# Kernel optimization log

Hardware: AMD Instinct MI355X
Metric: run time of the kernel (lower is better)

Reference implementation:

```python
import jax, jax.numpy as jnp
import numpy as np

EPS = 1e-6
GROUPS = 8


def setup_inputs() -> dict:
    key = jax.random.key(0)
    ks = jax.random.split(key, 8)
    B, C, H, W = 4, 128, 64, 64
    s = 1.0 / np.sqrt(C)
    return {
        "x": jax.random.normal(ks[0], (B, C, H, W), jnp.float32),
        "gn_scale": jnp.ones((C,), jnp.float32),
        "gn_bias": jnp.zeros((C,), jnp.float32),
        "wq": jax.random.normal(ks[1], (C, C), jnp.float32) * s,
        "bq": jnp.zeros((C,), jnp.float32),
        "wk": jax.random.normal(ks[2], (C, C), jnp.float32) * s,
        "bk": jnp.zeros((C,), jnp.float32),
        "wv": jax.random.normal(ks[3], (C, C), jnp.float32) * s,
        "bv": jnp.zeros((C,), jnp.float32),
        "wp": jax.random.normal(ks[4], (C, C), jnp.float32) * s,
        "bp": jnp.zeros((C,), jnp.float32),
    }


def _group_norm(x, scale, bias):
    B, C, H, W = x.shape
    g = x.reshape(B, GROUPS, C // GROUPS, H * W)
    mu = g.mean(axis=(2, 3), keepdims=True)
    var = g.var(axis=(2, 3), keepdims=True)
    g = (g - mu) * jax.lax.rsqrt(var + EPS)
    g = g.reshape(B, C, H, W)
    return g * scale[None, :, None, None] + bias[None, :, None, None]


def reference(x, gn_scale, gn_bias, wq, bq, wk, bk, wv, bv, wp, bp):
    B, C, H, W = x.shape
    N = H * W
    h = _group_norm(x, gn_scale, gn_bias).reshape(B, C, N)
    # 1x1 convs == channel matmuls: (C_out, C_in) x (B, C_in, N)
    q = jnp.einsum('oc,bcn->bon', wq, h) + bq[None, :, None]
    k = jnp.einsum('oc,bcn->bon', wk, h) + bk[None, :, None]
    v = jnp.einsum('oc,bcn->bon', wv, h) + bv[None, :, None]
    # scores: (B, N, N), w[b,n,m] = sum_c q[b,c,n] k[b,c,m]
    w = jnp.einsum('bcn,bcm->bnm', q, k) * (C ** -0.5)
    w = jax.nn.softmax(w, axis=-1)
    # h_[b,c,n] = sum_m w[b,n,m] v[b,c,m]
    h_ = jnp.einsum('bnm,bcm->bcn', w, v)
    out = jnp.einsum('oc,bcn->bon', wp, h_) + bp[None, :, None]
    return x + out.reshape(B, C, H, W)
```

## Files before the change

kernel.cpp:

```cpp
#include <hip/hip_runtime.h>
#include <math.h>

#define B_ 4
#define C_ 128
#define N_ 4096
#define NSPLIT 4
#define MT 32
#define PLD 40
#define HLD 136
#define VTLD 24

typedef float floatx4 __attribute__((ext_vector_type(4)));
typedef short bf16x8 __attribute__((ext_vector_type(8)));

__device__ __forceinline__ ushort f2bf(float f) {
  unsigned u = __float_as_uint(f);
  return (ushort)((u + 0x7FFF + ((u >> 16) & 1)) >> 16);
}
__device__ __forceinline__ float bf2f(ushort u) {
  return __uint_as_float(((unsigned)u) << 16);
}
__device__ __forceinline__ unsigned pkbf(float a, float b) {
  return __builtin_amdgcn_perm(__float_as_uint(a) + 0x8000u,
                               __float_as_uint(b) + 0x8000u, 0x07060302u);
}
__device__ __forceinline__ void gl2lds16(const ushort* g, ushort* l) {
  __builtin_amdgcn_global_load_lds(
      (const __attribute__((address_space(1))) void*)g,
      (__attribute__((address_space(3))) void*)l, 16, 0, 0);
}

__global__ __launch_bounds__(256) void prep_kernel(
    const float* __restrict__ x, float* __restrict__ gstat,
    const float* __restrict__ wq, const float* __restrict__ wk,
    const float* __restrict__ wv, const float* __restrict__ wp,
    ushort* __restrict__ wB) {
  if (blockIdx.x >= 256) {
    int i = (blockIdx.x - 256) * 256 + threadIdx.x;
    int m = i >> 14, j = i & 16383;
    const float* src = (m == 0) ? wq : (m == 1) ? wk : (m == 2) ? wv : wp;
    wB[i] = f2bf(src[j]);
    return;
  }
  int b = blockIdx.x >> 6, g = (blockIdx.x >> 3) & 7, part = blockIdx.x & 7;
  const float4* xp = (const float4*)(x + (size_t)(b * C_ + g * 16) * N_) + part * 2048;
  float s = 0.f, ss = 0.f;
  for (int i = threadIdx.x; i < 2048; i += 256) {
    float4 v = xp[i];
    s += v.x + v.y + v.z + v.w;
    ss += v.x * v.x + v.y * v.y + v.z * v.z + v.w * v.w;
  }
  #pragma unroll
  for (int o = 32; o > 0; o >>= 1) {
    s += __shfl_down(s, o, 64);
    ss += __shfl_down(ss, o, 64);
  }
  __shared__ float rs[4], rss[4];
  int wid = threadIdx.x >> 6, lane = threadIdx.x & 63;
  if (lane == 0) { rs[wid] = s; rss[wid] = ss; }
  __syncthreads();
  if (threadIdx.x == 0) {
    int slot = (b * 8 + g) * 8 + part;
    gstat[slot]       = rs[0] + rs[1] + rs[2] + rs[3];
    gstat[256 + slot] = rss[0] + rss[1] + rss[2] + rss[3];
  }
}

__global__ __launch_bounds__(256) void gnqkv_kernel(
    const float* __restrict__ x, const float* __restrict__ gstat,
    const float* __restrict__ scale, const float* __restrict__ bias,
    const ushort* __restrict__ wB,
    const float* __restrict__ bq, const float* __restrict__ bk,
    const float* __restrict__ bv,
    ushort* __restrict__ qT, ushort* __restrict__ kT, ushort* __restrict__ vB) {
  __shared__ __align__(16) ushort hs[16][HLD];
  __shared__ __align__(16) ushort Qt[16][HLD];
  __shared__ __align__(16) ushort Kt[16][HLD];
  __shared__ __align__(16) ushort Vt[128][VTLD];
  __shared__ float sSc[C_], sBi[C_];
  int tid = threadIdx.x;
  int b = blockIdx.x >> 8;
  int n0 = (blockIdx.x & 255) * 16;
  if (tid < 128) {
    int g = tid >> 4;
    float S = 0.f, SS = 0.f;
    #pragma unroll
    for (int p = 0; p < 8; ++p) {
      S  += gstat[(b * 8 + g) * 8 + p];
      SS += gstat[256 + (b * 8 + g) * 8 + p];
    }
    float mu = S * (1.f / 65536.f);
    float var = SS * (1.f / 65536.f) - mu * mu;
    float rstd = rsqrtf(var + 1e-6f);
    float sc = scale[tid] * rstd;
    sSc[tid] = sc;
    sBi[tid] = bias[tid] - mu * sc;
  }
  __syncthreads();
  #pragma unroll
  for (int k2 = 0; k2 < 2; ++k2) {
    int i = tid + k2 * 256;
    int c = i >> 2, n4 = i & 3;
    float4 v = *(const float4*)(x + (size_t)(b * C_ + c) * N_ + n0 + n4 * 4);
    float sc = sSc[c], bi = sBi[c];
    hs[n4 * 4 + 0][c] = f2bf(v.x * sc + bi);
    hs[n4 * 4 + 1][c] = f2bf(v.y * sc + bi);
    hs[n4 * 4 + 2][c] = f2bf(v.z * sc + bi);
    hs[n4 * 4 + 3][c] = f2bf(v.w * sc + bi);
  }
  __syncthreads();
  int lane = tid & 63, w = tid >> 6;
  int col = lane & 15, quad = lane >> 4;
  int oh = w * 32;
  bf16x8 hf[4];
  #pragma unroll
  for (int kc = 0; kc < 4; ++kc)
    hf[kc] = *(const bf16x8*)&hs[col][kc * 32 + quad * 8];
  const ushort* Wq = wB;
  const ushort* Wk = wB + 16384;
  const ushort* Wv = wB + 32768;
  const float scl = 0.12751879752224991f;
  #pragma unroll
  for (int ot = 0; ot < 2; ++ot) {
    int o0 = oh + ot * 16;
    floatx4 aq = (floatx4)0.f, ak = (floatx4)0.f, av = (floatx4)0.f;
    #pragma unroll
    for (int kc = 0; kc < 4; ++kc) {
      int wo = (o0 + col) * C_ + kc * 32 + quad * 8;
      aq = __builtin_amdgcn_mfma_f32_16x16x32_bf16(*(const bf16x8*)&Wq[wo], hf[kc], aq, 0, 0, 0);
      ak = __builtin_amdgcn_mfma_f32_16x16x32_bf16(*(const bf16x8*)&Wk[wo], hf[kc], ak, 0, 0, 0);
      av = __builtin_amdgcn_mfma_f32_16x16x32_bf16(*(const bf16x8*)&Wv[wo], hf[kc], av, 0, 0, 0);
    }
    float4 bqv = *(const float4*)&bq[o0 + quad * 4];
    float4 bkv = *(const float4*)&bk[o0 + quad * 4];
    float4 bvv = *(const float4*)&bv[o0 + quad * 4];
    uint2 qs = { pkbf((aq[1] + bqv.y) * scl, (aq[0] + bqv.x) * scl),
                 pkbf((aq[3] + bqv.w) * scl, (aq[2] + bqv.z) * scl) };
    uint2 ks = { pkbf(ak[1] + bkv.y, ak[0] + bkv.x),
                 pkbf(ak[3] + bkv.w, ak[2] + bkv.z) };
    *(uint2*)&Qt[col][o0 + quad * 4] = qs;
    *(uint2*)&Kt[col][o0 + quad * 4] = ks;
    float vv[4] = {av[0] + bvv.x, av[1] + bvv.y, av[2] + bvv.z, av[3] + bvv.w};
    #pragma unroll
    for (int r = 0; r < 4; ++r)
      Vt[o0 + quad * 4 + r][col] = f2bf(vv[r]);
  }
  __syncthreads();
  {
    int row = tid >> 4, seg = tid & 15;
    size_t dst = ((size_t)b * N_ + n0 + row) * C_ + seg * 8;
    *(uint4*)(qT + dst) = *(const uint4*)&Qt[row][seg * 8];
    *(uint4*)(kT + dst) = *(const uint4*)&Kt[row][seg * 8];
  }
  {
    int o = tid >> 1, seg = tid & 1;
    *(uint4*)(vB + ((size_t)b * C_ + o) * N_ + n0 + seg * 8) = *(const uint4*)&Vt[o][seg * 8];
  }
}

__global__ __launch_bounds__(256, 4) void attn_kernel(
    const ushort* __restrict__ qT, const ushort* __restrict__ kT,
    const ushort* __restrict__ vB, ushort* __restrict__ Op,
    float* __restrict__ Lv) {
  __shared__ __align__(16) ushort Ks[2][MT * 128];
  __shared__ __align__(16) ushort Vs[2][C_ * MT];
  __shared__ __align__(16) ushort Ps[64 * PLD];
  int qblk = blockIdx.x & 63;
  int sp = (blockIdx.x >> 6) & 3;
  int b = blockIdx.x >> 8;
  int n0 = qblk * 64;
  int tid = threadIdx.x, lane = tid & 63, w = tid >> 6;
  int col = lane & 15, quad = lane >> 4;
  int wu = __builtin_amdgcn_readfirstlane(w);
  const ushort* kTb = kT + (size_t)b * N_ * C_;
  const ushort* vBb = vB + (size_t)b * C_ * N_;

  bf16x8 qf[4];
  #pragma unroll
  for (int kc = 0; kc < 4; ++kc)
    qf[kc] = *(const bf16x8*)(qT + ((size_t)b * N_ + n0 + w * 16 + col) * C_ + kc * 32 + quad * 8);

  floatx4 Oacc[8];
  #pragma unroll
  for (int ct = 0; ct < 8; ++ct) Oacc[ct] = (floatx4)0.f;
  float lacc = 0.f;

  #define STAGE(m0v, buf)                                                              \
    {                                                                                  \
      _Pragma("unroll")                                                                \
      for (int j = 0; j < 2; ++j) {                                                    \
        int inst = wu * 2 + j;                                                         \
        int r = inst * 4 + (lane >> 4);                                                \
        int pos = (lane & 15) ^ (r & 7);                                               \
        gl2lds16(kTb + (size_t)((m0v) + r) * 128 + pos * 8, &Ks[buf][inst * 512]);     \
      }                                                                                \
      _Pragma("unroll")                                                                \
      for (int j = 0; j < 2; ++j) {                                                    \
        int inst = wu * 2 + j;                                                         \
        int c = inst * 16 + (lane >> 2);                                               \
        gl2lds16(vBb + (size_t)c * N_ + (m0v) + (lane & 3) * 8, &Vs[buf][inst * 512]); \
      }                                                                                \
    }

  STAGE(sp * 1024, 0);
  __syncthreads();

  for (int it = 0; it < 1024 / MT; ++it) {
    if (it < 1024 / MT - 1) STAGE(sp * 1024 + (it + 1) * MT, (it + 1) & 1);
    const ushort* KsB = Ks[it & 1];
    const ushort* VsB = Vs[it & 1];

    floatx4 st[2];
    #pragma unroll
    for (int mt = 0; mt < 2; ++mt) {
      int row = mt * 16 + col;
      bf16x8 kf[4];
      #pragma unroll
      for (int kc = 0; kc < 4; ++kc)
        kf[kc] = *(const bf16x8*)&KsB[row * 128 + (((4 * kc + quad) ^ (col & 7)) * 8)];
      floatx4 acc = (floatx4)0.f;
      #pragma unroll
      for (int kc = 0; kc < 4; ++kc)
        acc = __builtin_amdgcn_mfma_f32_16x16x32_bf16(kf[kc], qf[kc], acc, 0, 0, 0);
      st[mt] = acc;
    }
    int prow = (w * 16 + col) * PLD;
    #pragma unroll
    for (int mt = 0; mt < 2; ++mt) {
      float p0 = exp2f(st[mt][0]);
      float p1 = exp2f(st[mt][1]);
      float p2 = exp2f(st[mt][2]);
      float p3 = exp2f(st[mt][3]);
      uint2 pk = { pkbf(p1, p0), pkbf(p3, p2) };
      *(uint2*)&Ps[prow + mt * 16 + quad * 4] = pk;
      lacc += (p0 + p1) + (p2 + p3);
    }
    bf16x8 pf = *(const bf16x8*)&Ps[prow + quad * 8];
    #pragma unroll
    for (int ct = 0; ct < 8; ++ct) {
      bf16x8 vf = *(const bf16x8*)&VsB[(ct * 16 + col) * MT + quad * 8];
      Oacc[ct] = __builtin_amdgcn_mfma_f32_16x16x32_bf16(pf, vf, Oacc[ct], 0, 0, 0);
    }
    __syncthreads();
  }

  ushort* OpB = Op + (((size_t)sp * B_ + b) * N_ + n0 + w * 16) * C_;
  #pragma unroll
  for (int ct = 0; ct < 8; ++ct)
    #pragma unroll
    for (int r = 0; r < 4; ++r)
      OpB[(size_t)(quad * 4 + r) * C_ + ct * 16 + col] = f2bf(Oacc[ct][r]);
  float lsum = lacc;
  lsum += __shfl_xor(lsum, 16, 64);
  lsum += __shfl_xor(lsum, 32, 64);
  if (quad == 0) {
    int idx = b * N_ + n0 + w * 16 + col;
    Lv[(size_t)sp * (B_ * N_) + idx] = lsum;
  }
}

__global__ __launch_bounds__(256) void mergeproj_kernel(
    const ushort* __restrict__ Op, const float* __restrict__ Lv,
    const ushort* __restrict__ wpB, const float* __restrict__ bp,
    const float* __restrict__ x, float* __restrict__ out) {
  __shared__ __align__(16) ushort tile[16 * HLD];
  int tid = threadIdx.x;
  int b = blockIdx.x >> 8;
  int n0 = (blockIdx.x & 255) * 16;
  {
    int n = tid >> 4, cc = tid & 15;
    int nIdx = b * N_ + n0 + n;
    float den = Lv[0 * (B_ * N_) + nIdx] + Lv[1 * (B_ * N_) + nIdx] +
                Lv[2 * (B_ * N_) + nIdx] + Lv[3 * (B_ * N_) + nIdx];
    float inv = 1.f / den;
    float o[8];
    #pragma unroll
    for (int j = 0; j < 8; ++j) o[j] = 0.f;
    #pragma unroll
    for (int sp = 0; sp < NSPLIT; ++sp) {
      uint4 d = *(const uint4*)&Op[((size_t)sp * (B_ * N_) + nIdx) * C_ + cc * 8];
      unsigned dd[4] = {d.x, d.y, d.z, d.w};
      #pragma unroll
      for (int j = 0; j < 4; ++j) {
        o[j * 2]     += bf2f((ushort)(dd[j] & 0xFFFF));
        o[j * 2 + 1] += bf2f((ushort)(dd[j] >> 16));
      }
    }
    uint4 res;
    res.x = pkbf(o[1] * inv, o[0] * inv);
    res.y = pkbf(o[3] * inv, o[2] * inv);
    res.z = pkbf(o[5] * inv, o[4] * inv);
    res.w = pkbf(o[7] * inv, o[6] * inv);
    *(uint4*)&tile[n * HLD + cc * 8] = res;
  }
  __syncthreads();
  int lane = tid & 63, w = tid >> 6;
  int col = lane & 15, quad = lane >> 4;
  int oh = w * 32;
  bf16x8 hf[4];
  #pragma unroll
  for (int kc = 0; kc < 4; ++kc)
    hf[kc] = *(const bf16x8*)&tile[col * HLD + kc * 32 + quad * 8];
  #pragma unroll
  for (int ot = 0; ot < 2; ++ot) {
    int o0 = oh + ot * 16;
    floatx4 acc = (floatx4)0.f;
    #pragma unroll
    for (int kc = 0; kc < 4; ++kc) {
      int wo = (o0 + col) * C_ + kc * 32 + quad * 8;
      acc = __builtin_amdgcn_mfma_f32_16x16x32_bf16(*(const bf16x8*)&wpB[wo], hf[kc], acc, 0, 0, 0);
    }
    float4 bpv = *(const float4*)&bp[o0 + quad * 4];
    float bb[4] = {bpv.x, bpv.y, bpv.z, bpv.w};
    #pragma unroll
    for (int r = 0; r < 4; ++r) {
      size_t idx = ((size_t)b * C_ + o0 + quad * 4 + r) * N_ + n0 + col;
      out[idx] = acc[r] + bb[r] + x[idx];
    }
  }
}

extern "C" void kernel_launch(void* const* d_in, const int* in_sizes, int n_in,
                              void* d_out, int out_size, void* d_ws, size_t ws_size,
                              hipStream_t stream) {
  const float* x        = (const float*)d_in[0];
  const float* gn_scale = (const float*)d_in[1];
  const float* gn_bias  = (const float*)d_in[2];
  const float* wq = (const float*)d_in[3];
  const float* bq = (const float*)d_in[4];
  const float* wk = (const float*)d_in[5];
  const float* bk = (const float*)d_in[6];
  const float* wv = (const float*)d_in[7];
  const float* bv = (const float*)d_in[8];
  const float* wp = (const float*)d_in[9];
  const float* bp = (const float*)d_in[10];
  float* out = (float*)d_out;

  char* ws = (char*)d_ws;
  float*  Lv    = (float*)(ws + 262144);
  ushort* wB    = (ushort*)(ws + 524288);
  float*  gstat = (float*)(ws + 655360);
  ushort* qT    = (ushort*)(ws + (4u << 20));
  ushort* kT    = (ushort*)(ws + (8u << 20));
  ushort* vB    = (ushort*)(ws + (12u << 20));
  ushort* Op    = (ushort*)(ws + (16u << 20));
  ushort* wpB   = wB + 49152;

  prep_kernel<<<512, 256, 0, stream>>>(x, gstat, wq, wk, wv, wp, wB);
  gnqkv_kernel<<<1024, 256, 0, stream>>>(x, gstat, gn_scale, gn_bias, wB, bq, bk, bv, qT, kT, vB);
  attn_kernel<<<1024, 256, 0, stream>>>(qT, kT, vB, Op, Lv);
  mergeproj_kernel<<<1024, 256, 0, stream>>>(Op, Lv, wpB, bp, x, out);
}
```

Baseline: 158.2 us.

## Enlarge attention query tile to 128 rows and split PV by channel across waves

The attention kernel now handles 128 query rows per block instead of 64, with each wave computing scores for 32 queries. The P@V product is redistributed so each wave owns 32 output channels across all 128 queries, reading shared P from LDS. Each staged K/V tile is therefore reused across twice as many queries, which halves global K/V traffic and the number of blocks. The cost is more registers (occupancy hint drops from 4 to 3), an extra barrier per iteration, and fewer blocks to fill the GPU.

```diff
diff --git a/kernel.cpp b/kernel.cpp
--- a/kernel.cpp
+++ b/kernel.cpp
@@ -158,32 +158,36 @@
   }
 }
 
-__global__ __launch_bounds__(256, 4) void attn_kernel(
+__global__ __launch_bounds__(256, 3) void attn_kernel(
     const ushort* __restrict__ qT, const ushort* __restrict__ kT,
     const ushort* __restrict__ vB, ushort* __restrict__ Op,
     float* __restrict__ Lv) {
   __shared__ __align__(16) ushort Ks[2][MT * 128];
   __shared__ __align__(16) ushort Vs[2][C_ * MT];
-  __shared__ __align__(16) ushort Ps[64 * PLD];
-  int qblk = blockIdx.x & 63;
-  int sp = (blockIdx.x >> 6) & 3;
-  int b = blockIdx.x >> 8;
-  int n0 = qblk * 64;
+  __shared__ __align__(16) ushort Ps[128 * PLD];
+  int qblk = blockIdx.x & 31;
+  int sp = (blockIdx.x >> 5) & 3;
+  int b = blockIdx.x >> 7;
+  int n0 = qblk * 128;
   int tid = threadIdx.x, lane = tid & 63, w = tid >> 6;
   int col = lane & 15, quad = lane >> 4;
   int wu = __builtin_amdgcn_readfirstlane(w);
   const ushort* kTb = kT + (size_t)b * N_ * C_;
   const ushort* vBb = vB + (size_t)b * C_ * N_;
 
-  bf16x8 qf[4];
-  #pragma unroll
-  for (int kc = 0; kc < 4; ++kc)
-    qf[kc] = *(const bf16x8*)(qT + ((size_t)b * N_ + n0 + w * 16 + col) * C_ + kc * 32 + quad * 8);
-
-  floatx4 Oacc[8];
-  #pragma unroll
-  for (int ct = 0; ct < 8; ++ct) Oacc[ct] = (floatx4)0.f;
-  float lacc = 0.f;
+  bf16x8 qf[2][4];
+  #pragma unroll
+  for (int qt = 0; qt < 2; ++qt)
+    #pragma unroll
+    for (int kc = 0; kc < 4; ++kc)
+      qf[qt][kc] = *(const bf16x8*)(qT + ((size_t)b * N_ + n0 + w * 32 + qt * 16 + col) * C_ + kc * 32 + quad * 8);
+
+  floatx4 Oacc[8][2];
+  #pragma unroll
+  for (int qt = 0; qt < 8; ++qt)
+    #pragma unroll
+    for (int ct = 0; ct < 2; ++ct) Oacc[qt][ct] = (floatx4)0.f;
+  float lacc[2] = {0.f, 0.f};
 
   #define STAGE(m0v, buf)                                                              \
     {                                                                                  \
@@ -210,7 +214,7 @@
     const ushort* KsB = Ks[it & 1];
     const ushort* VsB = Vs[it & 1];
 
-    floatx4 st[2];
+    floatx4 st[2][2];
     #pragma unroll
     for (int mt = 0; mt < 2; ++mt) {
       int row = mt * 16 + col;
@@ -218,44 +222,59 @@
       #pragma unroll
       for (int kc = 0; kc < 4; ++kc)
         kf[kc] = *(const bf16x8*)&KsB[row * 128 + (((4 * kc + quad) ^ (col & 7)) * 8)];
-      floatx4 acc = (floatx4)0.f;
-      #pragma unroll
-      for (int kc = 0; kc < 4; ++kc)
-        acc = __builtin_amdgcn_mfma_f32_16x16x32_bf16(kf[kc], qf[kc], acc, 0, 0, 0);
-      st[mt] = acc;
-    }
-    int prow = (w * 16 + col) * PLD;
-    #pragma unroll
-    for (int mt = 0; mt < 2; ++mt) {
-      float p0 = exp2f(st[mt][0]);
-      float p1 = exp2f(st[mt][1]);
-      float p2 = exp2f(st[mt][2]);
-      float p3 = exp2f(st[mt][3]);
-      uint2 pk = { pkbf(p1, p0), pkbf(p3, p2) };
-      *(uint2*)&Ps[prow + mt * 16 + quad * 4] = pk;
-      lacc += (p0 + p1) + (p2 + p3);
-    }
-    bf16x8 pf = *(const bf16x8*)&Ps[prow + quad * 8];
-    #pragma unroll
-    for (int ct = 0; ct < 8; ++ct) {
-      bf16x8 vf = *(const bf16x8*)&VsB[(ct * 16 + col) * MT + quad * 8];
-      Oacc[ct] = __builtin_amdgcn_mfma_f32_16x16x32_bf16(pf, vf, Oacc[ct], 0, 0, 0);
+      #pragma unroll
+      for (int qt = 0; qt < 2; ++qt) {
+        floatx4 acc = (floatx4)0.f;
+        #pragma unroll
+        for (int kc = 0; kc < 4; ++kc)
+          acc = __builtin_amdgcn_mfma_f32_16x16x32_bf16(kf[kc], qf[qt][kc], acc, 0, 0, 0);
+        st[qt][mt] = acc;
+      }
+    }
+    #pragma unroll
+    for (int qt = 0; qt < 2; ++qt) {
+      int prow = (w * 32 + qt * 16 + col) * PLD;
+      #pragma unroll
+      for (int mt = 0; mt < 2; ++mt) {
+        float p0 = exp2f(st[qt][mt][0]);
+        float p1 = exp2f(st[qt][mt][1]);
+        float p2 = exp2f(st[qt][mt][2]);
+        float p3 = exp2f(st[qt][mt][3]);
+        uint2 pk = { pkbf(p1, p0), pkbf(p3, p2) };
+        *(uint2*)&Ps[prow + mt * 16 + quad * 4] = pk;
+        lacc[qt] += (p0 + p1) + (p2 + p3);
+      }
     }
     __syncthreads();
-  }
-
-  ushort* OpB = Op + (((size_t)sp * B_ + b) * N_ + n0 + w * 16) * C_;
-  #pragma unroll
-  for (int ct = 0; ct < 8; ++ct)
-    #pragma unroll
-    for (int r = 0; r < 4; ++r)
-      OpB[(size_t)(quad * 4 + r) * C_ + ct * 16 + col] = f2bf(Oacc[ct][r]);
-  float lsum = lacc;
-  lsum += __shfl_xor(lsum, 16, 64);
-  lsum += __shfl_xor(lsum, 32, 64);
-  if (quad == 0) {
-    int idx = b * N_ + n0 + w * 16 + col;
-    Lv[(size_t)sp * (B_ * N_) + idx] = lsum;
+    #pragma unroll
+    for (int ct = 0; ct < 2; ++ct) {
+      bf16x8 vf = *(const bf16x8*)&VsB[(w * 32 + ct * 16 + col) * MT + quad * 8];
+      #pragma unroll
+      for (int qt = 0; qt < 8; ++qt) {
+        bf16x8 pf = *(const bf16x8*)&Ps[(qt * 16 + col) * PLD + quad * 8];
+        Oacc[qt][ct] = __builtin_amdgcn_mfma_f32_16x16x32_bf16(pf, vf, Oacc[qt][ct], 0, 0, 0);
+      }
+    }
+    __syncthreads();
+  }
+
+  ushort* OpB = Op + (((size_t)sp * B_ + b) * N_ + n0) * C_;
+  #pragma unroll
+  for (int qt = 0; qt < 8; ++qt)
+    #pragma unroll
+    for (int ct = 0; ct < 2; ++ct)
+      #pragma unroll
+      for (int r = 0; r < 4; ++r)
+        OpB[(size_t)(qt * 16 + quad * 4 + r) * C_ + w * 32 + ct * 16 + col] = f2bf(Oacc[qt][ct][r]);
+  #pragma unroll
+  for (int qt = 0; qt < 2; ++qt) {
+    float lsum = lacc[qt];
+    lsum += __shfl_xor(lsum, 16, 64);
+    lsum += __shfl_xor(lsum, 32, 64);
+    if (quad == 0) {
+      int idx = b * N_ + n0 + w * 32 + qt * 16 + col;
+      Lv[(size_t)sp * (B_ * N_) + idx] = lsum;
+    }
   }
 }
 
@@ -348,6 +367,6 @@
 
   prep_kernel<<<512, 256, 0, stream>>>(x, gstat, wq, wk, wv, wp, wB);
   gnqkv_kernel<<<1024, 256, 0, stream>>>(x, gstat, gn_scale, gn_bias, wB, bq, bk, bv, qT, kT, vB);
-  attn_kernel<<<1024, 256, 0, stream>>>(qT, kT, vB, Op, Lv);
+  attn_kernel<<<512, 256, 0, stream>>>(qT, kT, vB, Op, Lv);
   mergeproj_kernel<<<1024, 256, 0, stream>>>(Op, Lv, wpB, bp, x, out);
 }
```

Measured after the change: 154.8 us. 1.02x faster.
